# Kernel tuning notes

Hardware: AMD Instinct MI355X
Metric: run time of the kernel (lower is better)

## Reference

```python
import jax, jax.numpy as jnp
import numpy as np
import math, itertools


def _dct_consts():
    t = np.zeros((8, 8, 8, 8), dtype=np.float32)
    for x, y, u, v in itertools.product(range(8), repeat=4):
        t[x, y, u, v] = math.cos((2 * x + 1) * u * math.pi / 16) * math.cos((2 * y + 1) * v * math.pi / 16)
    alpha = np.array([1.0 / np.sqrt(2)] + [1.0] * 7, dtype=np.float32)
    scale = np.outer(alpha, alpha).astype(np.float32) * 0.25
    return jnp.asarray(t), jnp.asarray(scale)

_TENSOR, _SCALE = _dct_consts()


def setup_inputs() -> dict:
    key = jax.random.key(0)
    # 64 RGB 512x512 images unfolded into 8x8 blocks: [B, C, n_blocks, 8, 8]
    image = jax.random.uniform(key, (64, 3, 4096, 8, 8), dtype=jnp.float32) * 255.0
    return {"image": image}


def reference(image) -> jnp.ndarray:
    x = image - 128.0
    # tensordot(image, tensor, dims=2): contract last two spatial dims (x,y)
    # with basis -> frequency dims (u,v); then elementwise scale.
    out = _SCALE * jnp.einsum('...xy,xyuv->...uv', x, _TENSOR)
    return out.reshape(image.shape)
```

## Files before the change

### kernel.cpp

```cpp
#include <hip/hip_runtime.h>

#define DCT_ROWS \
  {1.0f,  0.98078528f,  0.92387953f,  0.83146961f,  0.70710678f,  0.55557023f,  0.38268343f,  0.19509032f}, \
  {1.0f,  0.83146961f,  0.38268343f, -0.19509032f, -0.70710678f, -0.98078528f, -0.92387953f, -0.55557023f}, \
  {1.0f,  0.55557023f, -0.38268343f, -0.98078528f, -0.70710678f,  0.19509032f,  0.92387953f,  0.83146961f}, \
  {1.0f,  0.19509032f, -0.92387953f, -0.55557023f,  0.70710678f,  0.83146961f, -0.38268343f, -0.98078528f}, \
  {1.0f, -0.19509032f, -0.92387953f,  0.55557023f,  0.70710678f, -0.83146961f, -0.38268343f,  0.98078528f}, \
  {1.0f, -0.55557023f, -0.38268343f,  0.98078528f, -0.70710678f, -0.19509032f,  0.92387953f, -0.83146961f}, \
  {1.0f, -0.83146961f,  0.38268343f,  0.19509032f, -0.70710678f,  0.98078528f, -0.92387953f,  0.55557023f}, \
  {1.0f, -0.98078528f,  0.92387953f, -0.83146961f,  0.70710678f, -0.55557023f,  0.38268343f, -0.19509032f}

__constant__ float gC[8][8] = { DCT_ROWS };

__global__ __launch_bounds__(256) void dct8x8_kernel(const float* __restrict__ in,
                                                     float* __restrict__ out,
                                                     int nthreads) {
    constexpr float Ch[8][8] = { DCT_ROWS };

    const int tid = blockIdx.x * 256 + threadIdx.x;
    if (tid >= nthreads) return;
    const int u = threadIdx.x & 7;

    const float4* p = reinterpret_cast<const float4*>(in) + (size_t)tid * 2;
    float4 v0 = p[0];
    float4 v1 = p[1];
    float a[8] = { v0.x - 128.0f, v0.y - 128.0f, v0.z - 128.0f, v0.w - 128.0f,
                   v1.x - 128.0f, v1.y - 128.0f, v1.z - 128.0f, v1.w - 128.0f };

    float r[8];
#pragma unroll
    for (int v = 0; v < 8; ++v) {
        float s = 0.0f;
#pragma unroll
        for (int y = 0; y < 8; ++y) s = fmaf(a[y], Ch[y][v], s);
        r[v] = s;
    }

    float Ccol[8];
#pragma unroll
    for (int x = 0; x < 8; ++x) Ccol[x] = gC[x][u];

    float o[8] = {0.0f, 0.0f, 0.0f, 0.0f, 0.0f, 0.0f, 0.0f, 0.0f};
#pragma unroll
    for (int x = 0; x < 8; ++x) {
#pragma unroll
        for (int v = 0; v < 8; ++v) {
            float rx = __shfl(r[v], x, 8);
            o[v] = fmaf(Ccol[x], rx, o[v]);
        }
    }

    const float su = (u == 0) ? 0.35355339059f : 0.5f;
#pragma unroll
    for (int v = 0; v < 8; ++v) {
        const float sv = (v == 0) ? 0.35355339059f : 0.5f;
        o[v] *= su * sv;
    }

    float4* q = reinterpret_cast<float4*>(out) + (size_t)tid * 2;
    q[0] = make_float4(o[0], o[1], o[2], o[3]);
    q[1] = make_float4(o[4], o[5], o[6], o[7]);
}

extern "C" void kernel_launch(void* const* d_in, const int* in_sizes, int n_in,
                              void* d_out, int out_size, void* d_ws, size_t ws_size,
                              hipStream_t stream) {
    const float* in = (const float*)d_in[0];
    float* out = (float*)d_out;
    const int n = in_sizes[0];
    const int nthreads = n / 8;
    const int grid = (nthreads + 255) / 256;
    hipLaunchKernelGGL(dct8x8_kernel, dim3(grid), dim3(256), 0, stream,
                       in, out, nthreads);
}
```

Measured before the change: 77.49 us.

## Use fast butterfly DCT with LDS transpose and nontemporal stores

Replaces the dense 8x8 matrix-multiply DCT with a factored butterfly 1D DCT applied first along columns. The intermediate results are transposed through padded shared memory instead of using wavefront shuffles. The -128 offset is folded into the DC term as a -1024 constant, and outputs are written with nontemporal stores. This cuts FMA and shuffle count in a memory-bound kernel, but adds strided column loads, LDS traffic and a block barrier.

```diff
diff --git a/kernel.cpp b/kernel.cpp
--- a/kernel.cpp
+++ b/kernel.cpp
@@ -1,65 +1,63 @@
 #include <hip/hip_runtime.h>
 
-#define DCT_ROWS \
-  {1.0f,  0.98078528f,  0.92387953f,  0.83146961f,  0.70710678f,  0.55557023f,  0.38268343f,  0.19509032f}, \
-  {1.0f,  0.83146961f,  0.38268343f, -0.19509032f, -0.70710678f, -0.98078528f, -0.92387953f, -0.55557023f}, \
-  {1.0f,  0.55557023f, -0.38268343f, -0.98078528f, -0.70710678f,  0.19509032f,  0.92387953f,  0.83146961f}, \
-  {1.0f,  0.19509032f, -0.92387953f, -0.55557023f,  0.70710678f,  0.83146961f, -0.38268343f, -0.98078528f}, \
-  {1.0f, -0.19509032f, -0.92387953f,  0.55557023f,  0.70710678f, -0.83146961f, -0.38268343f,  0.98078528f}, \
-  {1.0f, -0.55557023f, -0.38268343f,  0.98078528f, -0.70710678f, -0.19509032f,  0.92387953f, -0.83146961f}, \
-  {1.0f, -0.83146961f,  0.38268343f,  0.19509032f, -0.70710678f,  0.98078528f, -0.92387953f,  0.55557023f}, \
-  {1.0f, -0.98078528f,  0.92387953f, -0.83146961f,  0.70710678f, -0.55557023f,  0.38268343f, -0.19509032f}
+typedef float fx4 __attribute__((ext_vector_type(4)));
 
-__constant__ float gC[8][8] = { DCT_ROWS };
+__device__ __forceinline__ void dct8(const float a[8], float o[8]) {
+    const float s0 = a[0] + a[7], s1 = a[1] + a[6], s2 = a[2] + a[5], s3 = a[3] + a[4];
+    const float d0 = a[0] - a[7], d1 = a[1] - a[6], d2 = a[2] - a[5], d3 = a[3] - a[4];
+    const float ss0 = s0 + s3, ss1 = s1 + s2;
+    const float ds0 = s0 - s3, ds1 = s1 - s2;
+    o[0] = ss0 + ss1;
+    o[4] = 0.70710678f * (ss0 - ss1);
+    o[2] = fmaf(0.92387953f, ds0,  0.38268343f * ds1);
+    o[6] = fmaf(0.38268343f, ds0, -0.92387953f * ds1);
+    o[1] = fmaf(0.98078528f, d0, fmaf( 0.83146961f, d1, fmaf( 0.55557023f, d2,  0.19509032f * d3)));
+    o[3] = fmaf(0.83146961f, d0, fmaf(-0.19509032f, d1, fmaf(-0.98078528f, d2, -0.55557023f * d3)));
+    o[5] = fmaf(0.55557023f, d0, fmaf(-0.98078528f, d1, fmaf( 0.19509032f, d2,  0.83146961f * d3)));
+    o[7] = fmaf(0.19509032f, d0, fmaf(-0.55557023f, d1, fmaf( 0.83146961f, d2, -0.98078528f * d3)));
+}
 
 __global__ __launch_bounds__(256) void dct8x8_kernel(const float* __restrict__ in,
                                                      float* __restrict__ out,
                                                      int nthreads) {
-    constexpr float Ch[8][8] = { DCT_ROWS };
+    __shared__ float lds[256 * 9];
 
-    const int tid = blockIdx.x * 256 + threadIdx.x;
-    if (tid >= nthreads) return;
-    const int u = threadIdx.x & 7;
+    int tid = blockIdx.x * 256 + threadIdx.x;
+    if (tid >= nthreads) tid = nthreads - 1;
+    const int lane = threadIdx.x;
+    const int c = lane & 7;
+    const size_t blk = (size_t)(tid >> 3);
 
-    const float4* p = reinterpret_cast<const float4*>(in) + (size_t)tid * 2;
-    float4 v0 = p[0];
-    float4 v1 = p[1];
-    float a[8] = { v0.x - 128.0f, v0.y - 128.0f, v0.z - 128.0f, v0.w - 128.0f,
-                   v1.x - 128.0f, v1.y - 128.0f, v1.z - 128.0f, v1.w - 128.0f };
+    const float* bp = in + blk * 64 + c;
+    float a[8];
+#pragma unroll
+    for (int x = 0; x < 8; ++x) a[x] = bp[x * 8];
 
-    float r[8];
+    float B[8];
+    dct8(a, B);
+    B[0] -= 1024.0f;
+
 #pragma unroll
-    for (int v = 0; v < 8; ++v) {
-        float s = 0.0f;
+    for (int u = 0; u < 8; ++u) lds[lane * 9 + u] = B[u];
+    __syncthreads();
+
+    const int gbase = (lane & ~7) * 9;
+    float t[8];
 #pragma unroll
-        for (int y = 0; y < 8; ++y) s = fmaf(a[y], Ch[y][v], s);
-        r[v] = s;
-    }
+    for (int y = 0; y < 8; ++y) t[y] = lds[gbase + y * 9 + c];
 
-    float Ccol[8];
+    float o[8];
+    dct8(t, o);
+
+    const float su = (c == 0) ? 0.35355339059f : 0.5f;
 #pragma unroll
-    for (int x = 0; x < 8; ++x) Ccol[x] = gC[x][u];
+    for (int v = 0; v < 8; ++v) o[v] *= su * ((v == 0) ? 0.35355339059f : 0.5f);
 
-    float o[8] = {0.0f, 0.0f, 0.0f, 0.0f, 0.0f, 0.0f, 0.0f, 0.0f};
-#pragma unroll
-    for (int x = 0; x < 8; ++x) {
-#pragma unroll
-        for (int v = 0; v < 8; ++v) {
-            float rx = __shfl(r[v], x, 8);
-            o[v] = fmaf(Ccol[x], rx, o[v]);
-        }
-    }
-
-    const float su = (u == 0) ? 0.35355339059f : 0.5f;
-#pragma unroll
-    for (int v = 0; v < 8; ++v) {
-        const float sv = (v == 0) ? 0.35355339059f : 0.5f;
-        o[v] *= su * sv;
-    }
-
-    float4* q = reinterpret_cast<float4*>(out) + (size_t)tid * 2;
-    q[0] = make_float4(o[0], o[1], o[2], o[3]);
-    q[1] = make_float4(o[4], o[5], o[6], o[7]);
+    fx4 q0 = { o[0], o[1], o[2], o[3] };
+    fx4 q1 = { o[4], o[5], o[6], o[7] };
+    fx4* qp = reinterpret_cast<fx4*>(out) + (size_t)tid * 2;
+    __builtin_nontemporal_store(q0, qp);
+    __builtin_nontemporal_store(q1, qp + 1);
 }
 
 extern "C" void kernel_launch(void* const* d_in, const int* in_sizes, int n_in,
```

Result: slower. 85.31 us (+10.1%).

## Compute whole 8x8 DCT per thread with separable butterfly factorization

Applied to the files above, without the earlier changes.

Each thread now loads an entire 8x8 block and applies a fast butterfly 1D DCT to rows then columns, replacing per-row matrix FMAs and cross-lane shuffles. The -128 level shift is folded into a single correction of the DC coefficient. This cuts arithmetic and shuffle traffic, but makes each thread's loads strided across the wave and raises register use, which may hurt memory coalescing and occupancy on a bandwidth-bound kernel. The bounds check is removed, assuming the block count divides evenly.

```diff
diff --git a/kernel.cpp b/kernel.cpp
--- a/kernel.cpp
+++ b/kernel.cpp
@@ -1,65 +1,64 @@
 #include <hip/hip_runtime.h>
 
-#define DCT_ROWS \
-  {1.0f,  0.98078528f,  0.92387953f,  0.83146961f,  0.70710678f,  0.55557023f,  0.38268343f,  0.19509032f}, \
-  {1.0f,  0.83146961f,  0.38268343f, -0.19509032f, -0.70710678f, -0.98078528f, -0.92387953f, -0.55557023f}, \
-  {1.0f,  0.55557023f, -0.38268343f, -0.98078528f, -0.70710678f,  0.19509032f,  0.92387953f,  0.83146961f}, \
-  {1.0f,  0.19509032f, -0.92387953f, -0.55557023f,  0.70710678f,  0.83146961f, -0.38268343f, -0.98078528f}, \
-  {1.0f, -0.19509032f, -0.92387953f,  0.55557023f,  0.70710678f, -0.83146961f, -0.38268343f,  0.98078528f}, \
-  {1.0f, -0.55557023f, -0.38268343f,  0.98078528f, -0.70710678f, -0.19509032f,  0.92387953f, -0.83146961f}, \
-  {1.0f, -0.83146961f,  0.38268343f,  0.19509032f, -0.70710678f,  0.98078528f, -0.92387953f,  0.55557023f}, \
-  {1.0f, -0.98078528f,  0.92387953f, -0.83146961f,  0.70710678f, -0.55557023f,  0.38268343f, -0.19509032f}
+typedef float fx4 __attribute__((ext_vector_type(4)));
 
-__constant__ float gC[8][8] = { DCT_ROWS };
+template <int S>
+__device__ __forceinline__ void dct8s(float* m) {
+    const float a0 = m[0*S], a1 = m[1*S], a2 = m[2*S], a3 = m[3*S];
+    const float a4 = m[4*S], a5 = m[5*S], a6 = m[6*S], a7 = m[7*S];
+    const float s0 = a0 + a7, s1 = a1 + a6, s2 = a2 + a5, s3 = a3 + a4;
+    const float d0 = a0 - a7, d1 = a1 - a6, d2 = a2 - a5, d3 = a3 - a4;
+    const float ss0 = s0 + s3, ss1 = s1 + s2;
+    const float ds0 = s0 - s3, ds1 = s1 - s2;
+    m[0*S] = ss0 + ss1;
+    m[4*S] = 0.70710678f * (ss0 - ss1);
+    m[2*S] = fmaf(0.92387953f, ds0,  0.38268343f * ds1);
+    m[6*S] = fmaf(0.38268343f, ds0, -0.92387953f * ds1);
+    m[1*S] = fmaf(0.98078528f, d0, fmaf( 0.83146961f, d1, fmaf( 0.55557023f, d2,  0.19509032f * d3)));
+    m[3*S] = fmaf(0.83146961f, d0, fmaf(-0.19509032f, d1, fmaf(-0.98078528f, d2, -0.55557023f * d3)));
+    m[5*S] = fmaf(0.55557023f, d0, fmaf(-0.98078528f, d1, fmaf( 0.19509032f, d2,  0.83146961f * d3)));
+    m[7*S] = fmaf(0.19509032f, d0, fmaf(-0.55557023f, d1, fmaf( 0.83146961f, d2, -0.98078528f * d3)));
+}
 
 __global__ __launch_bounds__(256) void dct8x8_kernel(const float* __restrict__ in,
-                                                     float* __restrict__ out,
-                                                     int nthreads) {
-    constexpr float Ch[8][8] = { DCT_ROWS };
+                                                     float* __restrict__ out) {
+    const size_t t = (size_t)blockIdx.x * 256 + threadIdx.x;
+    const fx4* p = reinterpret_cast<const fx4*>(in) + t * 16;
 
-    const int tid = blockIdx.x * 256 + threadIdx.x;
-    if (tid >= nthreads) return;
-    const int u = threadIdx.x & 7;
-
-    const float4* p = reinterpret_cast<const float4*>(in) + (size_t)tid * 2;
-    float4 v0 = p[0];
-    float4 v1 = p[1];
-    float a[8] = { v0.x - 128.0f, v0.y - 128.0f, v0.z - 128.0f, v0.w - 128.0f,
-                   v1.x - 128.0f, v1.y - 128.0f, v1.z - 128.0f, v1.w - 128.0f };
-
-    float r[8];
+    float m[64];
 #pragma unroll
-    for (int v = 0; v < 8; ++v) {
-        float s = 0.0f;
-#pragma unroll
-        for (int y = 0; y < 8; ++y) s = fmaf(a[y], Ch[y][v], s);
-        r[v] = s;
+    for (int i = 0; i < 16; ++i) {
+        fx4 v = p[i];
+        m[i * 4 + 0] = v[0];
+        m[i * 4 + 1] = v[1];
+        m[i * 4 + 2] = v[2];
+        m[i * 4 + 3] = v[3];
     }
 
-    float Ccol[8];
 #pragma unroll
-    for (int x = 0; x < 8; ++x) Ccol[x] = gC[x][u];
+    for (int r = 0; r < 8; ++r) dct8s<1>(&m[r * 8]);
 
-    float o[8] = {0.0f, 0.0f, 0.0f, 0.0f, 0.0f, 0.0f, 0.0f, 0.0f};
 #pragma unroll
-    for (int x = 0; x < 8; ++x) {
+    for (int c = 0; c < 8; ++c) dct8s<8>(&m[c]);
+
+    m[0] -= 8192.0f;
+
+#pragma unroll
+    for (int u = 0; u < 8; ++u) {
+        const float su = (u == 0) ? 0.35355339059f : 0.5f;
 #pragma unroll
         for (int v = 0; v < 8; ++v) {
-            float rx = __shfl(r[v], x, 8);
-            o[v] = fmaf(Ccol[x], rx, o[v]);
+            const float sv = (v == 0) ? 0.35355339059f : 0.5f;
+            m[u * 8 + v] *= su * sv;
         }
     }
 
-    const float su = (u == 0) ? 0.35355339059f : 0.5f;
+    fx4* q = reinterpret_cast<fx4*>(out) + t * 16;
 #pragma unroll
-    for (int v = 0; v < 8; ++v) {
-        const float sv = (v == 0) ? 0.35355339059f : 0.5f;
-        o[v] *= su * sv;
+    for (int i = 0; i < 16; ++i) {
+        fx4 v = { m[i * 4 + 0], m[i * 4 + 1], m[i * 4 + 2], m[i * 4 + 3] };
+        q[i] = v;
     }
-
-    float4* q = reinterpret_cast<float4*>(out) + (size_t)tid * 2;
-    q[0] = make_float4(o[0], o[1], o[2], o[3]);
-    q[1] = make_float4(o[4], o[5], o[6], o[7]);
 }
 
 extern "C" void kernel_launch(void* const* d_in, const int* in_sizes, int n_in,
@@ -68,8 +67,8 @@
     const float* in = (const float*)d_in[0];
     float* out = (float*)d_out;
     const int n = in_sizes[0];
-    const int nthreads = n / 8;
-    const int grid = (nthreads + 255) / 256;
+    const int nblocks = n / 64;
+    const int grid = nblocks / 256;
     hipLaunchKernelGGL(dct8x8_kernel, dim3(grid), dim3(256), 0, stream,
-                       in, out, nthreads);
+                       in, out);
 }
```

Result: slower. 129.3 us (+66.9%).
